# Kernel tuning notes

Hardware: AMD Instinct MI355X
Metric: run time of the kernel (lower is better)

## Reference

```python
import jax, jax.numpy as jnp
import numpy as np

EPS = 1e-5
LEAKY = 0.2


def _wn(v, g):
    # weight norm over all dims except output-channel dim 0 (torch default dim=0)
    return g * v / jnp.sqrt(jnp.sum(v * v, axis=(1, 2), keepdims=True))


def _conv1d(x_bsc, w, b):
    # x_bsc: [B,S,C_in]; w: [C_out,C_in,3]; kernel 3, stride 1, pad 1
    x = x_bsc.transpose(0, 2, 1)  # NCH
    y = jax.lax.conv_general_dilated(x, w, (1,), [(1, 1)],
                                     dimension_numbers=("NCH", "OIH", "NCH"))
    y = y + b[None, :, None]
    return y.transpose(0, 2, 1)


def _adain(x, style, lengths, proj_w, proj_b):
    # masked per-(sample,channel) instance norm over valid length, then style affine, then mask
    B, S, H = x.shape
    hs = style @ proj_w.T + proj_b            # [B, 2H]
    gamma, beta = hs[:, :H], hs[:, H:]
    mask = (jnp.arange(S)[None, :] < lengths[:, None]).astype(x.dtype)[..., None]  # [B,S,1]
    cnt = lengths.astype(x.dtype)[:, None, None]
    mean = jnp.sum(x * mask, axis=1, keepdims=True) / cnt
    var = jnp.sum(jnp.square(x - mean) * mask, axis=1, keepdims=True) / cnt  # biased, as F.instance_norm
    xn = (x - mean) * jax.lax.rsqrt(var + EPS)
    out = ((1.0 + gamma[:, None, :]) * xn + beta[:, None, :]) * mask
    return out, mask


def setup_inputs() -> dict:
    key = jax.random.key(0)
    ks = jax.random.split(key, 12)
    B, S, H, STY = 8, 2048, 512, 128
    inp = {
        "hidden_states": jax.random.normal(ks[0], (B, S, H), jnp.float32),
        "style": jax.random.normal(ks[1], (B, STY), jnp.float32),
        "input_lengths": jax.random.randint(ks[2], (B,), S // 2, S + 1, jnp.int32),
        # AdaIN projections (torch Linear: [out,in])
        "proj1_w": jax.random.normal(ks[3], (2 * H, STY), jnp.float32) * 0.02,
        "proj1_b": jnp.zeros((2 * H,), jnp.float32),
        "proj2_w": jax.random.normal(ks[4], (2 * H, STY), jnp.float32) * 0.02,
        "proj2_b": jnp.zeros((2 * H,), jnp.float32),
        # weight-normed conv1 / conv2: v [out,in,3], g [out,1,1], bias [out]
        "conv1_v": jax.random.normal(ks[5], (H, H, 3), jnp.float32) * 0.02,
        "conv1_g": jnp.ones((H, 1, 1), jnp.float32),
        "conv1_b": jnp.zeros((H,), jnp.float32),
        "conv2_v": jax.random.normal(ks[6], (H, H, 3), jnp.float32) * 0.02,
        "conv2_g": jnp.ones((H, 1, 1), jnp.float32),
        "conv2_b": jnp.zeros((H,), jnp.float32),
    }
    return inp


def reference(hidden_states, style, input_lengths,
              proj1_w, proj1_b, proj2_w, proj2_b,
              conv1_v, conv1_g, conv1_b, conv2_v, conv2_g, conv2_b):
    w1 = _wn(conv1_v, conv1_g)
    w2 = _wn(conv2_v, conv2_g)
    # residual branch
    h, mask = _adain(hidden_states, style, input_lengths, proj1_w, proj1_b)
    h = jnp.where(h >= 0, h, LEAKY * h)
    h = _conv1d(h, w1, conv1_b) * mask
    h, _ = _adain(h, style, input_lengths, proj2_w, proj2_b)
    h = jnp.where(h >= 0, h, LEAKY * h)
    h = _conv1d(h, w2, conv2_b) * mask
    # shortcut is identity (no upsample, no learned shortcut)
    return (h + hidden_states) / jnp.sqrt(jnp.asarray(2.0, hidden_states.dtype))
```

## Files before the change

kernel.cpp:

```cpp
#include <hip/hip_runtime.h>

#define NB 8
#define SS 2048
#define HH 512
#define NSTY 128
#define SP (SS + 2)
#define EPSF 1e-5f

#define BM 128
#define BN 128

typedef __attribute__((ext_vector_type(8))) short short8;
typedef __attribute__((ext_vector_type(4))) float floatx4;
typedef __attribute__((ext_vector_type(4))) unsigned short u16x4;
typedef unsigned short u16;

__device__ __forceinline__ float bf2f(u16 u) {
  union { float f; unsigned int i; } v; v.i = ((unsigned int)u) << 16; return v.f;
}
__device__ __forceinline__ u16 f2bf(float f) {
  union { float f; unsigned int i; } v; v.f = f;
  unsigned int x = v.i;
  return (u16)((x + 0x7fffu + ((x >> 16) & 1u)) >> 16);
}
__device__ __forceinline__ float lrelu(float v) { return v >= 0.f ? v : 0.2f * v; }

__device__ __forceinline__ void gld_lds16(const u16* g, u16* l) {
  __builtin_amdgcn_global_load_lds((const __attribute__((address_space(1))) void*)g,
                                   (__attribute__((address_space(3))) void*)l, 16, 0, 0);
}

__global__ void k_zero(float* p, int n) {
  int i = blockIdx.x * 256 + threadIdx.x;
  if (i < n) p[i] = 0.f;
}

__global__ void k_proj(const float* style, const float* w1, const float* b1,
                       const float* w2, const float* b2,
                       float* g1, float* be1, float* g2, float* be2) {
  int idx = blockIdx.x * 256 + threadIdx.x;
  if (idx >= 2 * NB * 2 * HH) return;
  int which = idx / (NB * 2 * HH);
  int r = idx % (NB * 2 * HH);
  int b = r / (2 * HH);
  int j = r % (2 * HH);
  const float* w = which ? w2 : w1;
  const float* bias = which ? b2 : b1;
  float acc = bias[j];
  const float* st = style + b * NSTY;
  const float* wr = w + j * NSTY;
  for (int t = 0; t < NSTY; t++) acc += st[t] * wr[t];
  float* gd = which ? g2 : g1;
  float* bd = which ? be2 : be1;
  if (j < HH) gd[b * HH + j] = acc;
  else        bd[b * HH + (j - HH)] = acc;
}

__global__ void k_wnorm(const float* v1, const float* g1, const float* v2, const float* g2,
                        u16* wt1, u16* wt2) {
  int o = blockIdx.x % HH;
  int which = blockIdx.x / HH;
  const float* v = which ? v2 : v1;
  const float* g = which ? g2 : g1;
  u16* wt = which ? wt2 : wt1;
  float s = 0.f;
  for (int e = threadIdx.x; e < HH * 3; e += 256) {
    float x = v[o * HH * 3 + e];
    s += x * x;
  }
  for (int off = 32; off > 0; off >>= 1) s += __shfl_down(s, off, 64);
  __shared__ float red[4];
  int wid = threadIdx.x >> 6, lane = threadIdx.x & 63;
  if (lane == 0) red[wid] = s;
  __syncthreads();
  float tot = red[0] + red[1] + red[2] + red[3];
  float scale = g[o] / sqrtf(tot);
  for (int e = threadIdx.x; e < HH * 3; e += 256) {
    int i = e / 3, k = e % 3;
    wt[(k * HH + o) * HH + i] = f2bf(v[o * HH * 3 + e] * scale);
  }
}

#define SSPLIT1 64
__global__ void k_stats_f32(const float* __restrict__ x, const int* __restrict__ lens,
                            float* __restrict__ sum, float* __restrict__ sumsq) {
  int b = blockIdx.x & 7;
  int chunk = blockIdx.x >> 3;
  int s0 = chunk * (SS / SSPLIT1);
  int h4 = (threadIdx.x & 127) * 4;
  int sr = threadIdx.x >> 7;
  int len = lens[b];
  float4 sm = {0.f, 0.f, 0.f, 0.f}, sq = {0.f, 0.f, 0.f, 0.f};
#pragma unroll
  for (int i = 0; i < 16; i++) {
    int s = s0 + i * 2 + sr;
    float4 v = *(const float4*)(x + ((long)(b * SS + s)) * HH + h4);
    float m = (s < len) ? 1.f : 0.f;
    v.x *= m; v.y *= m; v.z *= m; v.w *= m;
    sm.x += v.x; sm.y += v.y; sm.z += v.z; sm.w += v.w;
    sq.x += v.x * v.x; sq.y += v.y * v.y; sq.z += v.z * v.z; sq.w += v.w * v.w;
  }
  atomicAdd(&sum[b * HH + h4 + 0], sm.x);
  atomicAdd(&sum[b * HH + h4 + 1], sm.y);
  atomicAdd(&sum[b * HH + h4 + 2], sm.z);
  atomicAdd(&sum[b * HH + h4 + 3], sm.w);
  atomicAdd(&sumsq[b * HH + h4 + 0], sq.x);
  atomicAdd(&sumsq[b * HH + h4 + 1], sq.y);
  atomicAdd(&sumsq[b * HH + h4 + 2], sq.z);
  atomicAdd(&sumsq[b * HH + h4 + 3], sq.w);
}

__device__ __forceinline__ void affine4(const float* sum, const float* sumsq,
                                        const float* gam, const float* bet,
                                        int b, int i, float cnt,
                                        float4& av, float4& cv) {
  float4 sm = *(const float4*)(sum + b * HH + i);
  float4 sq = *(const float4*)(sumsq + b * HH + i);
  float4 gv = *(const float4*)(gam + b * HH + i);
  float4 bv = *(const float4*)(bet + b * HH + i);
  float rc = 1.f / cnt;
  float mx = sm.x * rc, my = sm.y * rc, mz = sm.z * rc, mw = sm.w * rc;
  av.x = (1.f + gv.x) * rsqrtf(sq.x * rc - mx * mx + EPSF);
  av.y = (1.f + gv.y) * rsqrtf(sq.y * rc - my * my + EPSF);
  av.z = (1.f + gv.z) * rsqrtf(sq.z * rc - mz * mz + EPSF);
  av.w = (1.f + gv.w) * rsqrtf(sq.w * rc - mw * mw + EPSF);
  cv.x = bv.x - mx * av.x;
  cv.y = bv.y - my * av.y;
  cv.z = bv.z - mz * av.z;
  cv.w = bv.w - mw * av.w;
}

__global__ void k_prep_f32(const float* __restrict__ x,
                           const float* __restrict__ sum, const float* __restrict__ sumsq,
                           const float* __restrict__ gam, const float* __restrict__ bet,
                           const int* __restrict__ lens, u16* __restrict__ z) {
  int b = blockIdx.x & 7;
  int v = (blockIdx.x >> 3) * 256 + threadIdx.x;
  long off = (long)v * 4;
  int i = (int)(off % HH);
  int r = (int)(off / HH);
  int s = r - 1;
  int len = lens[b];
  u16x4 outv;
  if (s < 0 || s >= SS || s >= len) {
    outv = (u16x4){0, 0, 0, 0};
  } else {
    float4 av, cv;
    affine4(sum, sumsq, gam, bet, b, i, (float)len, av, cv);
    const float4 xv = *(const float4*)(x + ((long)(b * SS + s)) * HH + i);
    outv.x = f2bf(lrelu(av.x * xv.x + cv.x));
    outv.y = f2bf(lrelu(av.y * xv.y + cv.y));
    outv.z = f2bf(lrelu(av.z * xv.z + cv.z));
    outv.w = f2bf(lrelu(av.w * xv.w + cv.w));
  }
  *(u16x4*)(z + ((long)(b * SP + r)) * HH + i) = outv;
}

__global__ void k_prep_bf16(const u16* __restrict__ y,
                            const float* __restrict__ sum, const float* __restrict__ sumsq,
                            const float* __restrict__ gam, const float* __restrict__ bet,
                            const int* __restrict__ lens, u16* __restrict__ z) {
  int b = blockIdx.x & 7;
  int v = (blockIdx.x >> 3) * 256 + threadIdx.x;
  long off = (long)v * 4;
  int i = (int)(off % HH);
  int r = (int)(off / HH);
  int s = r - 1;
  int len = lens[b];
  u16x4 outv;
  if (s < 0 || s >= SS || s >= len) {
    outv = (u16x4){0, 0, 0, 0};
  } else {
    float4 av, cv;
    affine4(sum, sumsq, gam, bet, b, i, (float)len, av, cv);
    const u16x4 yv = *(const u16x4*)(y + ((long)(b * SS + s)) * HH + i);
    outv.x = f2bf(lrelu(av.x * bf2f(yv.x) + cv.x));
    outv.y = f2bf(lrelu(av.y * bf2f(yv.y) + cv.y));
    outv.z = f2bf(lrelu(av.z * bf2f(yv.z) + cv.z));
    outv.w = f2bf(lrelu(av.w * bf2f(yv.w) + cv.w));
  }
  *(u16x4*)(z + ((long)(b * SP + r)) * HH + i) = outv;
}

__global__ __launch_bounds__(512, 4) void k_conv(const u16* __restrict__ z,
                                                 const u16* __restrict__ wt,
                                                 const float* __restrict__ bias,
                                                 const int* __restrict__ lens,
                                                 u16* __restrict__ yout,
                                                 const float* __restrict__ resid,
                                                 float* __restrict__ fout,
                                                 float* __restrict__ sum,
                                                 float* __restrict__ sumsq) {
  __shared__ __align__(16) u16 L[2][2][2][BM * 32];

  int nwg = gridDim.x;
  int bid = blockIdx.x;
  int t = (bid & 7) * (nwg >> 3) + (bid >> 3);
  int bn0 = (t % (HH / BN)) * BN; t /= (HH / BN);
  int bm0 = (t % (SS / BM)) * BM; t /= (SS / BM);
  int b = t;

  int tid = threadIdx.x;
  int wave = tid >> 6, lane = tid & 63;
  int team = wave >> 2;
  int tw = wave & 3;
  int wr = tw >> 1, wc = tw & 1;
  int l15 = lane & 15, l4 = lane >> 4;

  int t256 = tid & 255;

  u16* A0 = &L[team][0][0][0];
  u16* B0 = &L[team][0][1][0];
  u16* A1 = &L[team][1][0][0];
  u16* B1 = &L[team][1][1][0];

  const u16* zb = z + (size_t)b * SP * HH;
  int len = lens[b];

  floatx4 acc[4][4] = {};

  auto stage = [&](u16* dA, u16* dB, int st) {
    int k0 = st * 32;
    const u16* wkb = wt + (size_t)(k0 >> 9) * HH * HH + (k0 & 511);
#pragma unroll
    for (int i = 0; i < 2; i++) {
      int g = i * 256 + t256;
      int line = g >> 3, pp = g & 7;
      int p = pp ^ (line & 7);
      int r = line * 2 + (p >> 2), s = p & 3;
      gld_lds16(zb + (size_t)(bm0 + r) * HH + k0 + s * 8, dA + g * 8);
    }
#pragma unroll
    for (int i = 0; i < 2; i++) {
      int g = i * 256 + t256;
      int line = g >> 3, pp = g & 7;
      int p = pp ^ (line & 7);
      int r = line * 2 + (p >> 2), s = p & 3;
      gld_lds16(wkb + (size_t)(bn0 + r) * HH + s * 8, dB + g * 8);
    }
  };

  auto compute = [&](const u16* sA, const u16* sB) {
    short8 afr[4], bfr[4];
#pragma unroll
    for (int i = 0; i < 4; i++) {
      int ar = wr * 64 + i * 16 + l15;
      afr[i] = *(const short8*)&sA[(ar >> 1) * 64 + ((((ar & 1) * 4 + l4) ^ ((ar >> 1) & 7)) * 8)];
    }
#pragma unroll
    for (int j = 0; j < 4; j++) {
      int br = wc * 64 + j * 16 + l15;
      bfr[j] = *(const short8*)&sB[(br >> 1) * 64 + ((((br & 1) * 4 + l4) ^ ((br >> 1) & 7)) * 8)];
    }
    __builtin_amdgcn_s_setprio(1);
#pragma unroll
    for (int am = 0; am < 4; am++)
#pragma unroll
      for (int bn = 0; bn < 4; bn++)
        acc[am][bn] = __builtin_amdgcn_mfma_f32_16x16x32_bf16(afr[am], bfr[bn], acc[am][bn], 0, 0, 0);
    __builtin_amdgcn_s_setprio(0);
  };

  int st0 = team * 24;
  stage(A0, B0, st0);
  for (int tp = 0; tp < 12; tp++) {
    stage(A1, B1, st0 + 2 * tp + 1);
    asm volatile("s_waitcnt vmcnt(4)" ::: "memory");
    __builtin_amdgcn_s_barrier();
    compute(A0, B0);
    __builtin_amdgcn_s_barrier();
    if (tp < 11) {
      stage(A0, B0, st0 + 2 * tp + 2);
      asm volatile("s_waitcnt vmcnt(4)" ::: "memory");
    } else {
      asm volatile("s_waitcnt vmcnt(0)" ::: "memory");
    }
    __builtin_amdgcn_s_barrier();
    compute(A1, B1);
    if (tp < 11) __builtin_amdgcn_s_barrier();
  }
  __syncthreads();

  floatx4* scr = (floatx4*)&L[0][0][0][0];
  floatx4* my = scr + (size_t)team * 2048;
  if (team == 0) {
#pragma unroll
    for (int am = 0; am < 4; am++) {
      my[(am * 2 + 0) * 256 + t256] = acc[am][2];
      my[(am * 2 + 1) * 256 + t256] = acc[am][3];
    }
  } else {
#pragma unroll
    for (int am = 0; am < 4; am++) {
      my[(am * 2 + 0) * 256 + t256] = acc[am][0];
      my[(am * 2 + 1) * 256 + t256] = acc[am][1];
    }
  }
  __syncthreads();
  const floatx4* other = scr + (size_t)(team ^ 1) * 2048;
  if (team == 0) {
#pragma unroll
    for (int am = 0; am < 4; am++) {
      acc[am][0] += other[(am * 2 + 0) * 256 + t256];
      acc[am][1] += other[(am * 2 + 1) * 256 + t256];
    }
  } else {
#pragma unroll
    for (int am = 0; am < 4; am++) {
      acc[am][2] += other[(am * 2 + 0) * 256 + t256];
      acc[am][3] += other[(am * 2 + 1) * 256 + t256];
    }
  }

#define EPI(BN) do {                                                         \
    int o = bn0 + wc * 64 + (BN) * 16 + l15;                                 \
    float bv = bias[o];                                                      \
    float psum = 0.f, psq = 0.f;                                             \
    _Pragma("unroll")                                                        \
    for (int am = 0; am < 4; am++) {                                         \
      _Pragma("unroll")                                                      \
      for (int r = 0; r < 4; r++) {                                          \
        int s = bm0 + wr * 64 + am * 16 + l4 * 4 + r;                        \
        float v = acc[am][BN][r] + bv;                                       \
        v = (s < len) ? v : 0.f;                                             \
        size_t off = ((size_t)(b * SS + s)) * HH + o;                        \
        if (fout) {                                                          \
          fout[off] = (v + resid[off]) * 0.70710678118654752f;               \
        } else {                                                             \
          yout[off] = f2bf(v);                                               \
          psum += v;                                                         \
          psq += v * v;                                                      \
        }                                                                    \
      }                                                                      \
    }                                                                        \
    if (sum) {                                                               \
      psum += __shfl_xor(psum, 16, 64);                                      \
      psum += __shfl_xor(psum, 32, 64);                                      \
      psq  += __shfl_xor(psq, 16, 64);                                       \
      psq  += __shfl_xor(psq, 32, 64);                                       \
      if (l4 == 0) {                                                         \
        atomicAdd(&sum[b * HH + o], psum);                                   \
        atomicAdd(&sumsq[b * HH + o], psq);                                  \
      }                                                                      \
    }                                                                        \
  } while (0)

  if (team == 0) { EPI(0); EPI(1); }
  else           { EPI(2); EPI(3); }
#undef EPI
}

extern "C" void kernel_launch(void* const* d_in, const int* in_sizes, int n_in,
                              void* d_out, int out_size, void* d_ws, size_t ws_size,
                              hipStream_t stream) {
  const float* x    = (const float*)d_in[0];
  const float* sty  = (const float*)d_in[1];
  const int*   lens = (const int*)d_in[2];
  const float* p1w  = (const float*)d_in[3];
  const float* p1b  = (const float*)d_in[4];
  const float* p2w  = (const float*)d_in[5];
  const float* p2b  = (const float*)d_in[6];
  const float* c1v  = (const float*)d_in[7];
  const float* c1g  = (const float*)d_in[8];
  const float* c1b  = (const float*)d_in[9];
  const float* c2v  = (const float*)d_in[10];
  const float* c2g  = (const float*)d_in[11];
  const float* c2b  = (const float*)d_in[12];
  float* out = (float*)d_out;

  char* ws = (char*)d_ws;
  size_t cur = 0;
  auto alloc = [&](size_t bytes) {
    void* p = ws + cur;
    cur += (bytes + 255) & ~(size_t)255;
    return p;
  };
  u16*   wt1  = (u16*)alloc((size_t)3 * HH * HH * 2);
  u16*   wt2  = (u16*)alloc((size_t)3 * HH * HH * 2);
  float* g1   = (float*)alloc(NB * HH * 4);
  float* be1  = (float*)alloc(NB * HH * 4);
  float* g2   = (float*)alloc(NB * HH * 4);
  float* be2  = (float*)alloc(NB * HH * 4);
  float* sum1 = (float*)alloc(NB * HH * 4);
  float* sq1  = (float*)alloc(NB * HH * 4);
  float* sum2 = (float*)alloc(NB * HH * 4);
  float* sq2  = (float*)alloc(NB * HH * 4);
  u16*   z1   = (u16*)alloc((size_t)NB * SP * HH * 2);
  u16*   y1   = (u16*)alloc((size_t)NB * SS * HH * 2);
  u16*   z2   = (u16*)alloc((size_t)NB * SP * HH * 2);

  const int CGRID = NB * (SS / BM) * (HH / BN);

  k_zero<<<(4 * NB * HH + 255) / 256, 256, 0, stream>>>(sum1, 4 * NB * HH);

  k_proj<<<(2 * NB * 2 * HH + 255) / 256, 256, 0, stream>>>(sty, p1w, p1b, p2w, p2b,
                                                            g1, be1, g2, be2);
  k_wnorm<<<2 * HH, 256, 0, stream>>>(c1v, c1g, c2v, c2g, wt1, wt2);

  k_stats_f32<<<NB * SSPLIT1, 256, 0, stream>>>(x, lens, sum1, sq1);

  k_prep_f32<<<NB * (SP * HH / 4 / 256), 256, 0, stream>>>(x, sum1, sq1, g1, be1,
                                                           lens, z1);

  k_conv<<<CGRID, 512, 0, stream>>>(z1, wt1, c1b, lens, y1,
                                    nullptr, nullptr, sum2, sq2);

  k_prep_bf16<<<NB * (SP * HH / 4 / 256), 256, 0, stream>>>(y1, sum2, sq2, g2, be2,
                                                            lens, z2);

  k_conv<<<CGRID, 512, 0, stream>>>(z2, wt2, c2b, lens, nullptr,
                                    x, out, nullptr, nullptr);
}
```

Measured before the change: 133.9 us.

## Merge setup kernels and replace double-buffered conv pipeline with single-buffer BK=64 loop

Merges the zeroing, style-projection and weight-norm kernels into one launch to cut launch overhead. The conv GEMM drops its double-buffered BK=32 LDS pipeline with explicit vmcnt waits for a simpler single-buffer loop with BK=64 tiles and a plain row-XOR swizzle. This halves the number of barrier rounds per K step. In exchange, global-to-LDS loads no longer overlap with MFMA compute, which can stall the matrix units.

```diff
diff --git a/kernel.cpp b/kernel.cpp
--- a/kernel.cpp
+++ b/kernel.cpp
@@ -9,6 +9,7 @@
 
 #define BM 128
 #define BN 128
+#define BK 64
 
 typedef __attribute__((ext_vector_type(8))) short short8;
 typedef __attribute__((ext_vector_type(4))) float floatx4;
@@ -30,54 +31,57 @@
                                    (__attribute__((address_space(3))) void*)l, 16, 0, 0);
 }
 
-__global__ void k_zero(float* p, int n) {
-  int i = blockIdx.x * 256 + threadIdx.x;
-  if (i < n) p[i] = 0.f;
-}
-
-__global__ void k_proj(const float* style, const float* w1, const float* b1,
-                       const float* w2, const float* b2,
-                       float* g1, float* be1, float* g2, float* be2) {
-  int idx = blockIdx.x * 256 + threadIdx.x;
-  if (idx >= 2 * NB * 2 * HH) return;
-  int which = idx / (NB * 2 * HH);
-  int r = idx % (NB * 2 * HH);
-  int b = r / (2 * HH);
-  int j = r % (2 * HH);
-  const float* w = which ? w2 : w1;
-  const float* bias = which ? b2 : b1;
-  float acc = bias[j];
-  const float* st = style + b * NSTY;
-  const float* wr = w + j * NSTY;
-  for (int t = 0; t < NSTY; t++) acc += st[t] * wr[t];
-  float* gd = which ? g2 : g1;
-  float* bd = which ? be2 : be1;
-  if (j < HH) gd[b * HH + j] = acc;
-  else        bd[b * HH + (j - HH)] = acc;
-}
-
-__global__ void k_wnorm(const float* v1, const float* g1, const float* v2, const float* g2,
-                        u16* wt1, u16* wt2) {
-  int o = blockIdx.x % HH;
-  int which = blockIdx.x / HH;
-  const float* v = which ? v2 : v1;
-  const float* g = which ? g2 : g1;
-  u16* wt = which ? wt2 : wt1;
-  float s = 0.f;
-  for (int e = threadIdx.x; e < HH * 3; e += 256) {
-    float x = v[o * HH * 3 + e];
-    s += x * x;
-  }
-  for (int off = 32; off > 0; off >>= 1) s += __shfl_down(s, off, 64);
-  __shared__ float red[4];
-  int wid = threadIdx.x >> 6, lane = threadIdx.x & 63;
-  if (lane == 0) red[wid] = s;
-  __syncthreads();
-  float tot = red[0] + red[1] + red[2] + red[3];
-  float scale = g[o] / sqrtf(tot);
-  for (int e = threadIdx.x; e < HH * 3; e += 256) {
-    int i = e / 3, k = e % 3;
-    wt[(k * HH + o) * HH + i] = f2bf(v[o * HH * 3 + e] * scale);
+__global__ void k_setup(const float* __restrict__ style,
+                        const float* __restrict__ p1w, const float* __restrict__ p1b,
+                        const float* __restrict__ p2w, const float* __restrict__ p2b,
+                        const float* __restrict__ c1v, const float* __restrict__ c1g,
+                        const float* __restrict__ c2v, const float* __restrict__ c2g,
+                        u16* __restrict__ wt1, u16* __restrict__ wt2,
+                        float* __restrict__ g1, float* __restrict__ be1,
+                        float* __restrict__ g2, float* __restrict__ be2,
+                        float* __restrict__ stats ) {
+  int bid = blockIdx.x;
+  if (bid < 2 * HH) {
+    int o = bid % HH;
+    int which = bid / HH;
+    const float* v = which ? c2v : c1v;
+    const float* g = which ? c2g : c1g;
+    u16* wt = which ? wt2 : wt1;
+    float s = 0.f;
+    for (int e = threadIdx.x; e < HH * 3; e += 256) {
+      float x = v[o * HH * 3 + e];
+      s += x * x;
+    }
+    for (int off = 32; off > 0; off >>= 1) s += __shfl_down(s, off, 64);
+    __shared__ float red[4];
+    int wid = threadIdx.x >> 6, lane = threadIdx.x & 63;
+    if (lane == 0) red[wid] = s;
+    __syncthreads();
+    float tot = red[0] + red[1] + red[2] + red[3];
+    float scale = g[o] / sqrtf(tot);
+    for (int e = threadIdx.x; e < HH * 3; e += 256) {
+      int i = e / 3, k = e % 3;
+      wt[(k * HH + o) * HH + i] = f2bf(v[o * HH * 3 + e] * scale);
+    }
+  } else if (bid < 2 * HH + 64) {
+    int idx = (bid - 2 * HH) * 256 + threadIdx.x;
+    int which = idx / (NB * 2 * HH);
+    int r = idx % (NB * 2 * HH);
+    int b = r / (2 * HH);
+    int j = r % (2 * HH);
+    const float* w = which ? p2w : p1w;
+    const float* bias = which ? p2b : p1b;
+    float acc = bias[j];
+    const float* st = style + b * NSTY;
+    const float* wr = w + j * NSTY;
+    for (int t = 0; t < NSTY; t++) acc += st[t] * wr[t];
+    float* gd = which ? g2 : g1;
+    float* bd = which ? be2 : be1;
+    if (j < HH) gd[b * HH + j] = acc;
+    else        bd[b * HH + (j - HH)] = acc;
+  } else {
+    int i = (bid - 2 * HH - 64) * 256 + threadIdx.x;
+    stats[i] = 0.f;
   }
 }
 
@@ -191,7 +195,7 @@
                                                  float* __restrict__ fout,
                                                  float* __restrict__ sum,
                                                  float* __restrict__ sumsq) {
-  __shared__ __align__(16) u16 L[2][2][2][BM * 32];
+  __shared__ __align__(16) u16 L[2][2][BM * BK];
 
   int nwg = gridDim.x;
   int bid = blockIdx.x;
@@ -208,80 +212,57 @@
   int l15 = lane & 15, l4 = lane >> 4;
 
   int t256 = tid & 255;
-
-  u16* A0 = &L[team][0][0][0];
-  u16* B0 = &L[team][0][1][0];
-  u16* A1 = &L[team][1][0][0];
-  u16* B1 = &L[team][1][1][0];
+  int trow = t256 >> 3;
+  int tslot = t256 & 7;
+
+  u16* LA = &L[team][0][0];
+  u16* LB = &L[team][1][0];
 
   const u16* zb = z + (size_t)b * SP * HH;
   int len = lens[b];
+  int kt0 = team * 12;
 
   floatx4 acc[4][4] = {};
 
-  auto stage = [&](u16* dA, u16* dB, int st) {
-    int k0 = st * 32;
+  for (int kt = 0; kt < 12; kt++) {
+    int k0 = (kt0 + kt) * BK;
     const u16* wkb = wt + (size_t)(k0 >> 9) * HH * HH + (k0 & 511);
 #pragma unroll
-    for (int i = 0; i < 2; i++) {
-      int g = i * 256 + t256;
-      int line = g >> 3, pp = g & 7;
-      int p = pp ^ (line & 7);
-      int r = line * 2 + (p >> 2), s = p & 3;
-      gld_lds16(zb + (size_t)(bm0 + r) * HH + k0 + s * 8, dA + g * 8);
-    }
-#pragma unroll
-    for (int i = 0; i < 2; i++) {
-      int g = i * 256 + t256;
-      int line = g >> 3, pp = g & 7;
-      int p = pp ^ (line & 7);
-      int r = line * 2 + (p >> 2), s = p & 3;
-      gld_lds16(wkb + (size_t)(bn0 + r) * HH + s * 8, dB + g * 8);
-    }
-  };
-
-  auto compute = [&](const u16* sA, const u16* sB) {
-    short8 afr[4], bfr[4];
-#pragma unroll
-    for (int i = 0; i < 4; i++) {
-      int ar = wr * 64 + i * 16 + l15;
-      afr[i] = *(const short8*)&sA[(ar >> 1) * 64 + ((((ar & 1) * 4 + l4) ^ ((ar >> 1) & 7)) * 8)];
-    }
-#pragma unroll
-    for (int j = 0; j < 4; j++) {
-      int br = wc * 64 + j * 16 + l15;
-      bfr[j] = *(const short8*)&sB[(br >> 1) * 64 + ((((br & 1) * 4 + l4) ^ ((br >> 1) & 7)) * 8)];
-    }
-    __builtin_amdgcn_s_setprio(1);
-#pragma unroll
-    for (int am = 0; am < 4; am++)
-#pragma unroll
-      for (int bn = 0; bn < 4; bn++)
-        acc[am][bn] = __builtin_amdgcn_mfma_f32_16x16x32_bf16(afr[am], bfr[bn], acc[am][bn], 0, 0, 0);
-    __builtin_amdgcn_s_setprio(0);
-  };
-
-  int st0 = team * 24;
-  stage(A0, B0, st0);
-  for (int tp = 0; tp < 12; tp++) {
-    stage(A1, B1, st0 + 2 * tp + 1);
-    asm volatile("s_waitcnt vmcnt(4)" ::: "memory");
-    __builtin_amdgcn_s_barrier();
-    compute(A0, B0);
-    __builtin_amdgcn_s_barrier();
-    if (tp < 11) {
-      stage(A0, B0, st0 + 2 * tp + 2);
-      asm volatile("s_waitcnt vmcnt(4)" ::: "memory");
-    } else {
-      asm volatile("s_waitcnt vmcnt(0)" ::: "memory");
-    }
-    __builtin_amdgcn_s_barrier();
-    compute(A1, B1);
-    if (tp < 11) __builtin_amdgcn_s_barrier();
-  }
-  __syncthreads();
-
-  floatx4* scr = (floatx4*)&L[0][0][0][0];
+    for (int rr = 0; rr < 4; rr++) {
+      int r = rr * 32 + trow;
+      int sc = (tslot ^ (r & 7)) * 8;
+      gld_lds16(zb + (size_t)(bm0 + r) * HH + k0 + sc, LA + rr * 2048 + t256 * 8);
+    }
+#pragma unroll
+    for (int rr = 0; rr < 4; rr++) {
+      int r = rr * 32 + trow;
+      int sc = (tslot ^ (r & 7)) * 8;
+      gld_lds16(wkb + (size_t)(bn0 + r) * HH + sc, LB + rr * 2048 + t256 * 8);
+    }
+    __syncthreads();
+#pragma unroll
+    for (int kk = 0; kk < 2; kk++) {
+      short8 afr[4], bfr[4];
+#pragma unroll
+      for (int i = 0; i < 4; i++) {
+        int ar = wr * 64 + i * 16 + l15;
+        afr[i] = *(const short8*)&LA[ar * BK + (((kk * 4 + l4) ^ (ar & 7)) * 8)];
+      }
+#pragma unroll
+      for (int j = 0; j < 4; j++) {
+        int br = wc * 64 + j * 16 + l15;
+        bfr[j] = *(const short8*)&LB[br * BK + (((kk * 4 + l4) ^ (br & 7)) * 8)];
+      }
+#pragma unroll
+      for (int am = 0; am < 4; am++)
+#pragma unroll
+        for (int bn = 0; bn < 4; bn++)
+          acc[am][bn] = __builtin_amdgcn_mfma_f32_16x16x32_bf16(afr[am], bfr[bn], acc[am][bn], 0, 0, 0);
+    }
+    __syncthreads();
+  }
+
+  floatx4* scr = (floatx4*)&L[0][0][0];
   floatx4* my = scr + (size_t)team * 2048;
   if (team == 0) {
 #pragma unroll
@@ -391,11 +372,9 @@
 
   const int CGRID = NB * (SS / BM) * (HH / BN);
 
-  k_zero<<<(4 * NB * HH + 255) / 256, 256, 0, stream>>>(sum1, 4 * NB * HH);
-
-  k_proj<<<(2 * NB * 2 * HH + 255) / 256, 256, 0, stream>>>(sty, p1w, p1b, p2w, p2b,
-                                                            g1, be1, g2, be2);
-  k_wnorm<<<2 * HH, 256, 0, stream>>>(c1v, c1g, c2v, c2g, wt1, wt2);
+  k_setup<<<2 * HH + 128, 256, 0, stream>>>(sty, p1w, p1b, p2w, p2b,
+                                            c1v, c1g, c2v, c2g,
+                                            wt1, wt2, g1, be1, g2, be2, sum1);
 
   k_stats_f32<<<NB * SSPLIT1, 256, 0, stream>>>(x, lens, sum1, sq1);
 
```

Result: faster. 114.3 us (-14.6%).
